# Performance work log

Hardware: AMD Instinct MI355X
Metric: run time of the kernel (lower is better)

## Reference

```python
import jax, jax.numpy as jnp
import numpy as np

D_MODEL = 1024
N_HEADS = 16
D_K = D_MODEL // N_HEADS
THETA = 10000.0
BATCH = 2
SEQ = 2048


def apply_rope(x, positions):
    # x: [B, H, S, d_k], positions: [S] int
    half = D_K // 2
    inv_freq = 1.0 / (THETA ** (jnp.arange(half, dtype=jnp.float32) * 2.0 / D_K))  # [half]
    ang = positions.astype(jnp.float32)[:, None] * inv_freq[None, :]  # [S, half]
    cos = jnp.cos(ang)
    sin = jnp.sin(ang)
    xr = x.reshape(x.shape[:-1] + (half, 2))
    x1, x2 = xr[..., 0], xr[..., 1]
    o1 = x1 * cos - x2 * sin
    o2 = x1 * sin + x2 * cos
    return jnp.stack([o1, o2], axis=-1).reshape(x.shape)


def setup_inputs() -> dict:
    key = jax.random.key(0)
    ks = jax.random.split(key, 5)
    scale = 1.0 / np.sqrt(D_MODEL)
    return {
        "x": jax.random.normal(ks[0], (BATCH, SEQ, D_MODEL), jnp.float32),
        "token_positions": jnp.arange(SEQ, dtype=jnp.int32),
        "Wq": jax.random.normal(ks[1], (D_MODEL, D_MODEL), jnp.float32) * scale,
        "Wk": jax.random.normal(ks[2], (D_MODEL, D_MODEL), jnp.float32) * scale,
        "Wv": jax.random.normal(ks[3], (D_MODEL, D_MODEL), jnp.float32) * scale,
        "Wo": jax.random.normal(ks[4], (D_MODEL, D_MODEL), jnp.float32) * scale,
    }


def reference(x, token_positions, Wq, Wk, Wv, Wo):
    B, S, _ = x.shape
    # projections (Linear with weight [out, in], no bias): y = x @ W^T
    def split_heads(t):
        return t.reshape(B, S, N_HEADS, D_K).transpose(0, 2, 1, 3)  # [B,H,S,d_k]

    Q = split_heads(x @ Wq.T)
    K = split_heads(x @ Wk.T)
    V = split_heads(x @ Wv.T)

    Q = apply_rope(Q, token_positions)
    K = apply_rope(K, token_positions)

    scores = jnp.einsum("bhqd,bhkd->bhqk", Q, K) / np.sqrt(D_K)
    causal = jnp.tril(jnp.ones((S, S), dtype=bool))
    scores = jnp.where(causal, scores, -jnp.inf)
    attn = jax.nn.softmax(scores, axis=-1)
    out = jnp.einsum("bhqk,bhkd->bhqd", attn, V)  # [B,H,S,d_k]
    out = out.transpose(0, 2, 1, 3).reshape(B, S, D_MODEL)
    return out @ Wo.T
```

## Files before the change

kernel.cpp:

```cpp
#include <hip/hip_runtime.h>
#include <hip/hip_bf16.h>


typedef __bf16 bf16x8 __attribute__((ext_vector_type(8)));
typedef __bf16 bf16x4 __attribute__((ext_vector_type(4)));
typedef float f32x4 __attribute__((ext_vector_type(4)));
typedef unsigned short ushort8 __attribute__((ext_vector_type(8)));

#define BATCH 2
#define SEQ 2048
#define NH 16
#define DK 64
#define DM 1024
#define BH (BATCH*NH)
#define M_TOT (BATCH*SEQ)
#define NQT (SEQ/64)

__device__ __forceinline__ void gload16(const void* g, void* l) {
    __builtin_amdgcn_global_load_lds((const __attribute__((address_space(1))) void*)g,
                                     (__attribute__((address_space(3))) void*)l, 16, 0, 0);
}

__global__ void cvt_kernel(const float* __restrict__ s, __bf16* __restrict__ d, int n) {
    int i = (blockIdx.x * blockDim.x + threadIdx.x) * 4;
    if (i >= n) return;
    float4 v = *(const float4*)(s + i);
    bf16x4 o;
    o[0] = (__bf16)v.x; o[1] = (__bf16)v.y; o[2] = (__bf16)v.z; o[3] = (__bf16)v.w;
    *(bf16x4*)(d + i) = o;
}

__global__ void cvt4_kernel(const float* __restrict__ s0, const float* __restrict__ s1,
                            const float* __restrict__ s2, const float* __restrict__ s3,
                            __bf16* __restrict__ d0, __bf16* __restrict__ d1,
                            __bf16* __restrict__ d2, __bf16* __restrict__ d3, int n) {
    const int z = blockIdx.y;
    const float* s = (z == 0) ? s0 : (z == 1) ? s1 : (z == 2) ? s2 : s3;
    __bf16* d = (z == 0) ? d0 : (z == 1) ? d1 : (z == 2) ? d2 : d3;
    int i = (blockIdx.x * blockDim.x + threadIdx.x) * 4;
    if (i >= n) return;
    float4 v = *(const float4*)(s + i);
    bf16x4 o;
    o[0] = (__bf16)v.x; o[1] = (__bf16)v.y; o[2] = (__bf16)v.z; o[3] = (__bf16)v.w;
    *(bf16x4*)(d + i) = o;
}

__device__ __forceinline__ void gemm_tile_compute(
    const __bf16* __restrict__ A, const __bf16* __restrict__ W,
    int m0, int n0, int K, __bf16* sA, __bf16* sB, f32x4 (&acc)[4][4])
{
    const int t = threadIdx.x;
    const int lane = t & 63, wid = t >> 6;
    const int wr = wid >> 1, wc = wid & 1;
    const int g = lane >> 4, l15 = lane & 15;

    f32x4 zero = {0.f, 0.f, 0.f, 0.f};
#pragma unroll
    for (int mt = 0; mt < 4; ++mt)
#pragma unroll
        for (int nt = 0; nt < 4; ++nt) acc[mt][nt] = zero;

    for (int k0 = 0; k0 < K; k0 += 32) {
        __syncthreads();
#pragma unroll
        for (int rnd = 0; rnd < 2; ++rnd) {
            int s = rnd * 256 + t;
            int row = s >> 2, ch = s & 3;
            __bf16* dstA = sA + (rnd * 256 + wid * 64) * 8;
            __bf16* dstB = sB + (rnd * 256 + wid * 64) * 8;
            gload16(A + (size_t)(m0 + row) * K + k0 + ch * 8, dstA);
            gload16(W + (size_t)(n0 + row) * K + k0 + ch * 8, dstB);
        }
        __syncthreads();
        bf16x8 af[4], bfr[4];
#pragma unroll
        for (int mt = 0; mt < 4; ++mt)
            af[mt] = *(const bf16x8*)&sA[(wr * 64 + mt * 16 + l15) * 32 + g * 8];
#pragma unroll
        for (int nt = 0; nt < 4; ++nt)
            bfr[nt] = *(const bf16x8*)&sB[(wc * 64 + nt * 16 + l15) * 32 + g * 8];
#pragma unroll
        for (int mt = 0; mt < 4; ++mt)
#pragma unroll
            for (int nt = 0; nt < 4; ++nt)
                acc[mt][nt] = __builtin_amdgcn_mfma_f32_16x16x32_bf16(af[mt], bfr[nt], acc[mt][nt], 0, 0, 0);
    }
}

__global__ __launch_bounds__(256) void gemm_qkv(
    const __bf16* __restrict__ xb,
    const __bf16* __restrict__ wq, const __bf16* __restrict__ wk, const __bf16* __restrict__ wv,
    __bf16* __restrict__ Qb, __bf16* __restrict__ Kb, __bf16* __restrict__ VTb)
{
    __shared__ __align__(16) __bf16 sA[128 * 32], sB[128 * 32];
    const int z = blockIdx.z;
    const __bf16* W = (z == 0) ? wq : ((z == 1) ? wk : wv);
    f32x4 acc[4][4];
    const int m0 = blockIdx.y * 128, n0 = blockIdx.x * 128;
    gemm_tile_compute(xb, W, m0, n0, DM, sA, sB, acc);

    const int t = threadIdx.x, lane = t & 63, wid = t >> 6;
    const int wr = wid >> 1, wc = wid & 1, g = lane >> 4, l15 = lane & 15;
    __bf16* QK = (z == 0) ? Qb : Kb;
#pragma unroll
    for (int mt = 0; mt < 4; ++mt)
#pragma unroll
        for (int nt = 0; nt < 4; ++nt)
#pragma unroll
            for (int r = 0; r < 4; ++r) {
                int m = m0 + wr * 64 + mt * 16 + g * 4 + r;
                int n = n0 + wc * 64 + nt * 16 + l15;
                int b = m >> 11, s = m & 2047, h = n >> 6, d = n & 63;
                __bf16 v = (__bf16)acc[mt][nt][r];
                if (z < 2)
                    QK[(((size_t)(b * NH + h)) * SEQ + s) * DK + d] = v;
                else
                    VTb[(((size_t)(b * NH + h)) * DK + d) * SEQ + s] = v;
            }
}

__global__ __launch_bounds__(256) void gemm_out(
    const __bf16* __restrict__ AO, const __bf16* __restrict__ wo, float* __restrict__ out)
{
    __shared__ __align__(16) __bf16 sA[128 * 32], sB[128 * 32];
    f32x4 acc[4][4];
    const int m0 = blockIdx.y * 128, n0 = blockIdx.x * 128;
    gemm_tile_compute(AO, wo, m0, n0, DM, sA, sB, acc);

    const int t = threadIdx.x, lane = t & 63, wid = t >> 6;
    const int wr = wid >> 1, wc = wid & 1, g = lane >> 4, l15 = lane & 15;
#pragma unroll
    for (int mt = 0; mt < 4; ++mt)
#pragma unroll
        for (int nt = 0; nt < 4; ++nt)
#pragma unroll
            for (int r = 0; r < 4; ++r) {
                int m = m0 + wr * 64 + mt * 16 + g * 4 + r;
                int n = n0 + wc * 64 + nt * 16 + l15;
                out[(size_t)m * DM + n] = acc[mt][nt][r];
            }
}

__global__ __launch_bounds__(256) void rope_kernel(
    __bf16* __restrict__ Qb, __bf16* __restrict__ Kb, const int* __restrict__ pos)
{
    __shared__ float ctab[32], stab[32];
    const int s = blockIdx.x;
    const int t = threadIdx.x;
    if (t < 32) {
        float invf = exp2f(-13.287712379549449f * (float)t * (1.0f / 32.0f));
        float ang = (float)pos[s] * invf;
        float sn, cs;
        sincosf(ang, &sn, &cs);
        ctab[t] = cs; stab[t] = sn;
    }
    __syncthreads();
#pragma unroll
    for (int u = 0; u < 8; ++u) {
        int id = u * 256 + t;
        int i = id & 31;
        int bh = (id >> 5) & 31;
        __bf16* P = (id >> 10) ? Kb : Qb;
        __bf16* p = P + ((size_t)bh * SEQ + s) * DK + i * 2;
        float x1 = (float)p[0], x2 = (float)p[1];
        float c = ctab[i], sn = stab[i];
        p[0] = (__bf16)(x1 * c - x2 * sn);
        p[1] = (__bf16)(x1 * sn + x2 * c);
    }
}

__global__ __launch_bounds__(256) void attn_kernel(
    const __bf16* __restrict__ Qb, const __bf16* __restrict__ Kb,
    const __bf16* __restrict__ VTb, __bf16* __restrict__ AO)
{
    __shared__ __align__(16) __bf16 sK[64 * 64];
    __shared__ __align__(16) __bf16 sV[64 * 64];
    __shared__ __align__(16) __bf16 sP[4 * 16 * 64];

    const int x = blockIdx.x, bh = blockIdx.y;
    const int t = threadIdx.x, lane = t & 63, wid = t >> 6;
    const int g = lane >> 4, l15 = lane & 15;

    const size_t baseQK = (size_t)bh * SEQ * DK;
    const size_t baseVT = (size_t)bh * DK * SEQ;
    const int b = bh >> 4, h = bh & 15;

    char* myP = (char*)(sP + wid * 16 * 64);
    f32x4 zero = {0.f, 0.f, 0.f, 0.f};

    for (int ph = 0; ph < 2; ++ph) {
        const int qt = ph ? (NQT - 1 - x) : x;

        bf16x8 qf[2];
        {
            const __bf16* qp = Qb + baseQK + (size_t)(qt * 64 + wid * 16 + l15) * DK;
            qf[0] = *(const bf16x8*)(qp + g * 8);
            qf[1] = *(const bf16x8*)(qp + 32 + g * 8);
        }

        f32x4 oacc[4];
#pragma unroll
        for (int dt = 0; dt < 4; ++dt) oacc[dt] = zero;
        float mrow[4], lrow[4];
#pragma unroll
        for (int r = 0; r < 4; ++r) { mrow[r] = -3e38f; lrow[r] = 0.f; }

        const char* Kt0 = (const char*)(Kb + baseQK);
        const char* Vt0 = (const char*)(VTb + baseVT);

        for (int kt = 0; kt <= qt; ++kt) {
            __syncthreads();
            const char* Kt = Kt0 + (size_t)kt * 64 * 128;
            const char* Vt = Vt0 + (size_t)kt * 128;
#pragma unroll
            for (int cc = 0; cc < 2; ++cc) {
                int c = t + cc * 256;
                int r = c >> 3, p = c & 7;
                int pp = p ^ (r & 7);
                *(ushort8*)((char*)sK + r * 128 + pp * 16) =
                    *(const ushort8*)(Kt + (size_t)r * 128 + p * 16);
                *(ushort8*)((char*)sV + r * 128 + pp * 16) =
                    *(const ushort8*)(Vt + (size_t)r * (SEQ * 2) + p * 16);
            }
            __syncthreads();

            f32x4 sacc[4];
#pragma unroll
            for (int nt = 0; nt < 4; ++nt) {
                sacc[nt] = zero;
#pragma unroll
                for (int ks = 0; ks < 2; ++ks) {
                    int row = nt * 16 + l15;
                    bf16x8 kf = *(const bf16x8*)((const char*)sK + row * 128 +
                                                 ((ks * 64 + g * 16) ^ ((row & 7) << 4)));
                    sacc[nt] = __builtin_amdgcn_mfma_f32_16x16x32_bf16(qf[ks], kf, sacc[nt], 0, 0, 0);
                }
            }
#pragma unroll
            for (int nt = 0; nt < 4; ++nt)
#pragma unroll
                for (int r = 0; r < 4; ++r) {
                    float sv = sacc[nt][r] * 0.125f;
                    if (kt == qt) {
                        int c_local = nt * 16 + l15;
                        int q_local = wid * 16 + g * 4 + r;
                        if (c_local > q_local) sv = -3e38f;
                    }
                    sacc[nt][r] = sv;
                }

#pragma unroll
            for (int r = 0; r < 4; ++r) {
                float tm = fmaxf(fmaxf(sacc[0][r], sacc[1][r]), fmaxf(sacc[2][r], sacc[3][r]));
#pragma unroll
                for (int msk = 1; msk < 16; msk <<= 1) tm = fmaxf(tm, __shfl_xor(tm, msk));
                float mnew = fmaxf(mrow[r], tm);
                float sc = __expf(mrow[r] - mnew);
                float rs = 0.f;
#pragma unroll
                for (int nt = 0; nt < 4; ++nt) {
                    float p = __expf(sacc[nt][r] - mnew);
                    sacc[nt][r] = p;
                    rs += p;
                }
#pragma unroll
                for (int msk = 1; msk < 16; msk <<= 1) rs += __shfl_xor(rs, msk);
                lrow[r] = lrow[r] * sc + rs;
                mrow[r] = mnew;
#pragma unroll
                for (int dt = 0; dt < 4; ++dt) oacc[dt][r] *= sc;
            }

#pragma unroll
            for (int nt = 0; nt < 4; ++nt)
#pragma unroll
                for (int r = 0; r < 4; ++r) {
                    int row = g * 4 + r;
                    *(__bf16*)(myP + row * 128 +
                               ((nt * 32 + l15 * 2) ^ ((row & 7) << 4))) = (__bf16)sacc[nt][r];
                }

#pragma unroll
            for (int ks = 0; ks < 2; ++ks) {
                bf16x8 pf = *(const bf16x8*)(myP + l15 * 128 +
                                             ((ks * 64 + g * 16) ^ ((l15 & 7) << 4)));
#pragma unroll
                for (int dt = 0; dt < 4; ++dt) {
                    int row = dt * 16 + l15;
                    bf16x8 vf = *(const bf16x8*)((const char*)sV + row * 128 +
                                                 ((ks * 64 + g * 16) ^ ((row & 7) << 4)));
                    oacc[dt] = __builtin_amdgcn_mfma_f32_16x16x32_bf16(pf, vf, oacc[dt], 0, 0, 0);
                }
            }
        }

#pragma unroll
        for (int r = 0; r < 4; ++r) {
            float inv = 1.0f / lrow[r];
            int srow = qt * 64 + wid * 16 + g * 4 + r;
            size_t obase = ((size_t)b * SEQ + srow) * DM + h * DK;
#pragma unroll
            for (int dt = 0; dt < 4; ++dt)
                AO[obase + dt * 16 + l15] = (__bf16)(oacc[dt][r] * inv);
        }
    }
}

extern "C" void kernel_launch(void* const* d_in, const int* in_sizes, int n_in,
                              void* d_out, int out_size, void* d_ws, size_t ws_size,
                              hipStream_t stream) {
    (void)in_sizes; (void)n_in; (void)out_size; (void)ws_size;
    const float* x  = (const float*)d_in[0];
    const int*  pos = (const int*)d_in[1];
    const float* Wq = (const float*)d_in[2];
    const float* Wk = (const float*)d_in[3];
    const float* Wv = (const float*)d_in[4];
    const float* Wo = (const float*)d_in[5];
    float* out = (float*)d_out;

    char* ws = (char*)d_ws;
    __bf16* xb  = (__bf16*)ws; ws += (size_t)M_TOT * DM * 2;
    __bf16* wqb = (__bf16*)ws; ws += (size_t)DM * DM * 2;
    __bf16* wkb = (__bf16*)ws; ws += (size_t)DM * DM * 2;
    __bf16* wvb = (__bf16*)ws; ws += (size_t)DM * DM * 2;
    __bf16* wob = (__bf16*)ws; ws += (size_t)DM * DM * 2;
    __bf16* Qb  = (__bf16*)ws; ws += (size_t)BH * SEQ * DK * 2;
    __bf16* Kb  = (__bf16*)ws; ws += (size_t)BH * SEQ * DK * 2;
    __bf16* VTb = (__bf16*)ws; ws += (size_t)BH * SEQ * DK * 2;
    __bf16* AOb = (__bf16*)ws; ws += (size_t)M_TOT * DM * 2;

    const int nx = M_TOT * DM, nw = DM * DM;
    cvt_kernel<<<nx / 4 / 256, 256, 0, stream>>>(x, xb, nx);
    cvt4_kernel<<<dim3(nw / 4 / 256, 4), 256, 0, stream>>>(Wq, Wk, Wv, Wo, wqb, wkb, wvb, wob, nw);

    gemm_qkv<<<dim3(DM / 128, M_TOT / 128, 3), 256, 0, stream>>>(xb, wqb, wkb, wvb, Qb, Kb, VTb);
    rope_kernel<<<SEQ, 256, 0, stream>>>(Qb, Kb, pos);
    attn_kernel<<<dim3(NQT / 2, BH), 256, 0, stream>>>(Qb, Kb, VTb, AOb);
    gemm_out<<<dim3(DM / 128, M_TOT / 128), 256, 0, stream>>>(AOb, wob, out);
}
```

Baseline: 229.4 us.

## Restructure attention: 128-row Q tiles, double-buffered async K/V loads, XCD-aware scheduling

```diff
diff --git a/kernel.cpp b/kernel.cpp
--- a/kernel.cpp
+++ b/kernel.cpp
@@ -14,7 +14,7 @@
 #define DM 1024
 #define BH (BATCH*NH)
 #define M_TOT (BATCH*SEQ)
-#define NQT (SEQ/64)
+#define QB 128
 
 __device__ __forceinline__ void gload16(const void* g, void* l) {
     __builtin_amdgcn_global_load_lds((const __attribute__((address_space(1))) void*)g,
@@ -169,141 +169,178 @@
     }
 }
 
-__global__ __launch_bounds__(256) void attn_kernel(
+__global__ __launch_bounds__(256, 3) void attn_kernel(
     const __bf16* __restrict__ Qb, const __bf16* __restrict__ Kb,
     const __bf16* __restrict__ VTb, __bf16* __restrict__ AO)
 {
-    __shared__ __align__(16) __bf16 sK[64 * 64];
-    __shared__ __align__(16) __bf16 sV[64 * 64];
-    __shared__ __align__(16) __bf16 sP[4 * 16 * 64];
-
-    const int x = blockIdx.x, bh = blockIdx.y;
+    __shared__ __align__(16) __bf16 sK[2][64 * 64];
+    __shared__ __align__(16) __bf16 sV[2][64 * 64];
+    __shared__ __align__(16) __bf16 sP[4 * 2 * 16 * 64];
+
+    const int n = blockIdx.x + 16 * blockIdx.y;
+    const int xcd = n & 7, slot = n >> 3;
+    const int bh = xcd * 4 + (slot >> 4);
+    const int j = 15 - (slot & 15);
     const int t = threadIdx.x, lane = t & 63, wid = t >> 6;
     const int g = lane >> 4, l15 = lane & 15;
 
     const size_t baseQK = (size_t)bh * SEQ * DK;
     const size_t baseVT = (size_t)bh * DK * SEQ;
     const int b = bh >> 4, h = bh & 15;
-
-    char* myP = (char*)(sP + wid * 16 * 64);
+    const int qrow_w = j * QB + wid * 32;
+
+    bf16x8 qf[2][2];
+#pragma unroll
+    for (int s = 0; s < 2; ++s) {
+        const __bf16* qp = Qb + baseQK + (size_t)(qrow_w + s * 16 + l15) * DK;
+        qf[s][0] = *(const bf16x8*)(qp + g * 8);
+        qf[s][1] = *(const bf16x8*)(qp + 32 + g * 8);
+    }
+
     f32x4 zero = {0.f, 0.f, 0.f, 0.f};
-
-    for (int ph = 0; ph < 2; ++ph) {
-        const int qt = ph ? (NQT - 1 - x) : x;
-
-        bf16x8 qf[2];
-        {
-            const __bf16* qp = Qb + baseQK + (size_t)(qt * 64 + wid * 16 + l15) * DK;
-            qf[0] = *(const bf16x8*)(qp + g * 8);
-            qf[1] = *(const bf16x8*)(qp + 32 + g * 8);
-        }
-
-        f32x4 oacc[4];
-#pragma unroll
-        for (int dt = 0; dt < 4; ++dt) oacc[dt] = zero;
-        float mrow[4], lrow[4];
-#pragma unroll
-        for (int r = 0; r < 4; ++r) { mrow[r] = -3e38f; lrow[r] = 0.f; }
-
-        const char* Kt0 = (const char*)(Kb + baseQK);
-        const char* Vt0 = (const char*)(VTb + baseVT);
-
-        for (int kt = 0; kt <= qt; ++kt) {
-            __syncthreads();
-            const char* Kt = Kt0 + (size_t)kt * 64 * 128;
-            const char* Vt = Vt0 + (size_t)kt * 128;
-#pragma unroll
-            for (int cc = 0; cc < 2; ++cc) {
-                int c = t + cc * 256;
-                int r = c >> 3, p = c & 7;
-                int pp = p ^ (r & 7);
-                *(ushort8*)((char*)sK + r * 128 + pp * 16) =
-                    *(const ushort8*)(Kt + (size_t)r * 128 + p * 16);
-                *(ushort8*)((char*)sV + r * 128 + pp * 16) =
-                    *(const ushort8*)(Vt + (size_t)r * (SEQ * 2) + p * 16);
-            }
-            __syncthreads();
-
-            f32x4 sacc[4];
-#pragma unroll
-            for (int nt = 0; nt < 4; ++nt) {
-                sacc[nt] = zero;
-#pragma unroll
-                for (int ks = 0; ks < 2; ++ks) {
-                    int row = nt * 16 + l15;
-                    bf16x8 kf = *(const bf16x8*)((const char*)sK + row * 128 +
-                                                 ((ks * 64 + g * 16) ^ ((row & 7) << 4)));
-                    sacc[nt] = __builtin_amdgcn_mfma_f32_16x16x32_bf16(qf[ks], kf, sacc[nt], 0, 0, 0);
-                }
-            }
-#pragma unroll
-            for (int nt = 0; nt < 4; ++nt)
-#pragma unroll
-                for (int r = 0; r < 4; ++r) {
-                    float sv = sacc[nt][r] * 0.125f;
-                    if (kt == qt) {
-                        int c_local = nt * 16 + l15;
-                        int q_local = wid * 16 + g * 4 + r;
-                        if (c_local > q_local) sv = -3e38f;
+    f32x4 oacc[2][4];
+    float mrow[2][4], lrow[2][4];
+#pragma unroll
+    for (int s = 0; s < 2; ++s)
+#pragma unroll
+        for (int r = 0; r < 4; ++r) {
+            oacc[s][r] = zero;
+        }
+#pragma unroll
+    for (int s = 0; s < 2; ++s)
+#pragma unroll
+        for (int dt = 0; dt < 4; ++dt) oacc[s][dt] = zero;
+#pragma unroll
+    for (int s = 0; s < 2; ++s)
+#pragma unroll
+        for (int r = 0; r < 4; ++r) { mrow[s][r] = -3e38f; lrow[s][r] = 0.f; }
+
+    const char* Kt0 = (const char*)(Kb + baseQK);
+    const char* Vt0 = (const char*)(VTb + baseVT);
+    const int ktmax = 2 * j + 1;
+
+    auto stage_tile = [&](int kt, int bq) {
+        const char* Kt = Kt0 + (size_t)kt * 64 * 128;
+        const char* Vt = Vt0 + (size_t)kt * 128;
+#pragma unroll
+        for (int cc = 0; cc < 2; ++cc) {
+            int c = t + cc * 256;
+            int r = c >> 3, pp = c & 7;
+            int p = pp ^ (r & 7);
+            char* bK = (char*)sK[bq] + (cc * 256 + wid * 64) * 16;
+            char* bV = (char*)sV[bq] + (cc * 256 + wid * 64) * 16;
+            gload16(Kt + (size_t)r * 128 + p * 16, bK);
+            gload16(Vt + (size_t)r * (SEQ * 2) + p * 16, bV);
+        }
+    };
+
+    stage_tile(0, 0);
+    __syncthreads();
+    int cur = 0;
+
+    for (int kt = 0; kt <= ktmax; ++kt) {
+        if (kt < ktmax) stage_tile(kt + 1, cur ^ 1);
+
+        f32x4 sacc[2][4];
+#pragma unroll
+        for (int s = 0; s < 2; ++s)
+#pragma unroll
+            for (int nt = 0; nt < 4; ++nt) sacc[s][nt] = zero;
+#pragma unroll
+        for (int nt = 0; nt < 4; ++nt) {
+            int row = nt * 16 + l15;
+#pragma unroll
+            for (int ks = 0; ks < 2; ++ks) {
+                bf16x8 kf = *(const bf16x8*)((const char*)sK[cur] + row * 128 +
+                                             ((ks * 64 + g * 16) ^ ((row & 7) << 4)));
+                sacc[0][nt] = __builtin_amdgcn_mfma_f32_16x16x32_bf16(qf[0][ks], kf, sacc[0][nt], 0, 0, 0);
+                sacc[1][nt] = __builtin_amdgcn_mfma_f32_16x16x32_bf16(qf[1][ks], kf, sacc[1][nt], 0, 0, 0);
+            }
+        }
+
+#pragma unroll
+        for (int s = 0; s < 2; ++s) {
+            const int q0 = qrow_w + s * 16;
+            if (kt * 64 + 63 > q0) {
+#pragma unroll
+                for (int nt = 0; nt < 4; ++nt)
+#pragma unroll
+                    for (int r = 0; r < 4; ++r) {
+                        int kv = kt * 64 + nt * 16 + l15;
+                        int q = q0 + g * 4 + r;
+                        if (kv > q) sacc[s][nt][r] = -3e38f; else sacc[s][nt][r] *= 0.125f;
                     }
-                    sacc[nt][r] = sv;
-                }
-
+            } else {
+#pragma unroll
+                for (int nt = 0; nt < 4; ++nt)
+#pragma unroll
+                    for (int r = 0; r < 4; ++r) sacc[s][nt][r] *= 0.125f;
+            }
 #pragma unroll
             for (int r = 0; r < 4; ++r) {
-                float tm = fmaxf(fmaxf(sacc[0][r], sacc[1][r]), fmaxf(sacc[2][r], sacc[3][r]));
+                float tm = fmaxf(fmaxf(sacc[s][0][r], sacc[s][1][r]),
+                                 fmaxf(sacc[s][2][r], sacc[s][3][r]));
 #pragma unroll
                 for (int msk = 1; msk < 16; msk <<= 1) tm = fmaxf(tm, __shfl_xor(tm, msk));
-                float mnew = fmaxf(mrow[r], tm);
-                float sc = __expf(mrow[r] - mnew);
+                float mnew = fmaxf(mrow[s][r], tm);
+                float sc = __expf(mrow[s][r] - mnew);
                 float rs = 0.f;
 #pragma unroll
                 for (int nt = 0; nt < 4; ++nt) {
-                    float p = __expf(sacc[nt][r] - mnew);
-                    sacc[nt][r] = p;
+                    float p = __expf(sacc[s][nt][r] - mnew);
+                    sacc[s][nt][r] = p;
                     rs += p;
                 }
 #pragma unroll
                 for (int msk = 1; msk < 16; msk <<= 1) rs += __shfl_xor(rs, msk);
-                lrow[r] = lrow[r] * sc + rs;
-                mrow[r] = mnew;
-#pragma unroll
-                for (int dt = 0; dt < 4; ++dt) oacc[dt][r] *= sc;
-            }
-
+                lrow[s][r] = lrow[s][r] * sc + rs;
+                mrow[s][r] = mnew;
+#pragma unroll
+                for (int dt = 0; dt < 4; ++dt) oacc[s][dt][r] *= sc;
+            }
+            char* myP = (char*)sP + (wid * 2 + s) * 2048;
 #pragma unroll
             for (int nt = 0; nt < 4; ++nt)
 #pragma unroll
                 for (int r = 0; r < 4; ++r) {
                     int row = g * 4 + r;
                     *(__bf16*)(myP + row * 128 +
-                               ((nt * 32 + l15 * 2) ^ ((row & 7) << 4))) = (__bf16)sacc[nt][r];
+                               ((nt * 32 + l15 * 2) ^ ((row & 7) << 4))) = (__bf16)sacc[s][nt][r];
                 }
-
-#pragma unroll
-            for (int ks = 0; ks < 2; ++ks) {
-                bf16x8 pf = *(const bf16x8*)(myP + l15 * 128 +
-                                             ((ks * 64 + g * 16) ^ ((l15 & 7) << 4)));
-#pragma unroll
-                for (int dt = 0; dt < 4; ++dt) {
-                    int row = dt * 16 + l15;
-                    bf16x8 vf = *(const bf16x8*)((const char*)sV + row * 128 +
-                                                 ((ks * 64 + g * 16) ^ ((row & 7) << 4)));
-                    oacc[dt] = __builtin_amdgcn_mfma_f32_16x16x32_bf16(pf, vf, oacc[dt], 0, 0, 0);
-                }
-            }
-        }
-
+        }
+
+#pragma unroll
+        for (int ks = 0; ks < 2; ++ks) {
+            bf16x8 pf[2];
+#pragma unroll
+            for (int s = 0; s < 2; ++s)
+                pf[s] = *(const bf16x8*)((char*)sP + (wid * 2 + s) * 2048 + l15 * 128 +
+                                         ((ks * 64 + g * 16) ^ ((l15 & 7) << 4)));
+#pragma unroll
+            for (int dt = 0; dt < 4; ++dt) {
+                int row = dt * 16 + l15;
+                bf16x8 vf = *(const bf16x8*)((const char*)sV[cur] + row * 128 +
+                                             ((ks * 64 + g * 16) ^ ((row & 7) << 4)));
+                oacc[0][dt] = __builtin_amdgcn_mfma_f32_16x16x32_bf16(pf[0], vf, oacc[0][dt], 0, 0, 0);
+                oacc[1][dt] = __builtin_amdgcn_mfma_f32_16x16x32_bf16(pf[1], vf, oacc[1][dt], 0, 0, 0);
+            }
+        }
+
+        __syncthreads();
+        cur ^= 1;
+    }
+
+#pragma unroll
+    for (int s = 0; s < 2; ++s)
 #pragma unroll
         for (int r = 0; r < 4; ++r) {
-            float inv = 1.0f / lrow[r];
-            int srow = qt * 64 + wid * 16 + g * 4 + r;
+            float inv = 1.0f / lrow[s][r];
+            int srow = qrow_w + s * 16 + g * 4 + r;
             size_t obase = ((size_t)b * SEQ + srow) * DM + h * DK;
 #pragma unroll
             for (int dt = 0; dt < 4; ++dt)
-                AO[obase + dt * 16 + l15] = (__bf16)(oacc[dt][r] * inv);
-        }
-    }
+                AO[obase + dt * 16 + l15] = (__bf16)(oacc[s][dt][r] * inv);
+        }
 }
 
 extern "C" void kernel_launch(void* const* d_in, const int* in_sizes, int n_in,
@@ -335,6 +372,6 @@
 
     gemm_qkv<<<dim3(DM / 128, M_TOT / 128, 3), 256, 0, stream>>>(xb, wqb, wkb, wvb, Qb, Kb, VTb);
     rope_kernel<<<SEQ, 256, 0, stream>>>(Qb, Kb, pos);
-    attn_kernel<<<dim3(NQT / 2, BH), 256, 0, stream>>>(Qb, Kb, VTb, AOb);
+    attn_kernel<<<dim3(16, BH), 256, 0, stream>>>(Qb, Kb, VTb, AOb);
     gemm_out<<<dim3(DM / 128, M_TOT / 128), 256, 0, stream>>>(AOb, wob, out);
 }
```

Measured after the change: 269.3 us. 1.17x slower.
